# Performance work log

Hardware: AMD Instinct MI355X
Metric: run time of the kernel (lower is better)

## Reference

```python
import math
import jax, jax.numpy as jnp
import numpy as np

H = 16  # head_count
D = 1024  # model_dim
DH = D // H  # dim_per_head = 64
PAD_IDX = 1


def setup_inputs() -> dict:
    key = jax.random.key(0)
    ks = jax.random.split(key, 16)
    B, L = 4, 512
    s = 0.02
    inp = {
        'key': jax.random.normal(ks[0], (B, L, D), jnp.float32),
        'value': jax.random.normal(ks[1], (B, L, D), jnp.float32),
        'query': jax.random.normal(ks[2], (B, L, D), jnp.float32),
        'ast_parents_matrix': jax.random.randint(ks[3], (B, L, L), 0, 200, jnp.int32),
        'mask': jnp.zeros((B, 1, L), jnp.bool_),
        'Wq': jax.random.normal(ks[4], (D, D), jnp.float32) * s,
        'bq': jnp.zeros((D,), jnp.float32),
        'Wk': jax.random.normal(ks[5], (D, D), jnp.float32) * s,
        'bk': jnp.zeros((D,), jnp.float32),
        'Wv': jax.random.normal(ks[6], (D, D), jnp.float32) * s,
        'bv': jnp.zeros((D,), jnp.float32),
        'Wo': jax.random.normal(ks[7], (D, D), jnp.float32) * s,
        'bo': jnp.zeros((D,), jnp.float32),
        'struct_emb': jax.random.normal(ks[8], (200, DH), jnp.float32).at[PAD_IDX].set(0.0),
        'value_emb': jax.random.normal(ks[9], (10000, DH), jnp.float32).at[PAD_IDX].set(0.0),
    }
    return inp


def _parent_embeddings(matrix, struct_emb, value_emb):
    # matrix: (B, Lq, K) int ids; even key positions use structure vocab, odd use value vocab
    B, Lq, K = matrix.shape
    s_ids = matrix[:, :, ::2]   # (B, Lq, ceil(K/2))
    v_ids = matrix[:, :, 1::2]  # (B, Lq, floor(K/2))
    emb_s = struct_emb[s_ids]   # (B, Lq, S, DH)
    emb_v = value_emb[v_ids]    # (B, Lq, V, DH)
    S = emb_s.shape[2]
    if emb_v.shape[2] != S:  # odd K: pad value stream by one zero slot, drop after interleave
        emb_v = jnp.concatenate([emb_v, jnp.zeros_like(emb_s[:, :, :1])], axis=2)
    pe = jnp.stack([emb_s, emb_v], axis=3).reshape(B, Lq, 2 * S, DH)
    return pe[:, :, :K, :]  # (B, Lq, K, DH)


def reference(key, value, query, ast_parents_matrix, mask,
              Wq, bq, Wk, bk, Wv, bv, Wo, bo, struct_emb, value_emb):
    B, L, _ = query.shape

    def shape(x):
        return x.reshape(B, -1, H, DH).transpose(0, 2, 1, 3)  # (B,H,L,DH)

    q = shape(query @ Wq + bq) / math.sqrt(DH)
    k = shape(key @ Wk + bk)
    v = shape(value @ Wv + bv)

    qk = jnp.einsum('bhid,bhjd->bhij', q, k)  # (B,H,L,L)

    pe = _parent_embeddings(ast_parents_matrix[:, :, :L], struct_emb, value_emb)
    score_ast = jnp.einsum('bhid,bijd->bhij', q, pe)

    scores = (qk + score_ast).astype(jnp.float32)
    scores = jnp.where(mask[:, None, :, :], -1e18, scores)  # mask: (B,1,L)->(B,1,1,L)
    attn = jax.nn.softmax(scores, axis=-1).astype(q.dtype)
    # dropout p=0.0 (eval) -> identity
    context = jnp.einsum('bhij,bhjd->bhid', attn, v)  # (B,H,L,DH)
    context = context.transpose(0, 2, 1, 3).reshape(B, L, D)
    output = context @ Wo + bo
    return output, attn
```

## Files before the change

kernel.cpp:

```cpp
#include <hip/hip_runtime.h>
#include <cstddef>

#define H 16
#define D 1024
#define DH 64
#define L 512

typedef __attribute__((ext_vector_type(8))) short bf16x8;
typedef __attribute__((ext_vector_type(4))) short bf16x4;
typedef __attribute__((ext_vector_type(4))) float f32x4;

__device__ inline short f2bf(float x) {
    union { float f; unsigned u; } c; c.f = x;
    unsigned r = (c.u + 0x7FFFu + ((c.u >> 16) & 1u)) >> 16;
    return (short)r;
}
__device__ inline float bf2f(short x) {
    union { float f; unsigned u; } c;
    c.u = ((unsigned)(unsigned short)x) << 16; return c.f;
}

__device__ inline void gload_lds16(const void* g, void* l) {
    __builtin_amdgcn_global_load_lds(
        (const __attribute__((address_space(1))) unsigned int*)g,
        (__attribute__((address_space(3))) unsigned int*)l,
        16, 0, 0);
}

struct PrepArgs {
    const float* csrc[5]; short* cdst[5]; int cn[5];
    const float* W[4]; short* T[4];
};

__global__ __launch_bounds__(256) void prep_kernel(PrepArgs a) {
    const int y = blockIdx.y;
    if (y < 5) {
        const float* s = a.csrc[y];
        short* d = a.cdst[y];
        int n = a.cn[y];
        int i = (blockIdx.x * 256 + threadIdx.x) * 8;
        if (i >= n) return;
        float4 x0 = *(const float4*)(s + i);
        float4 x1 = *(const float4*)(s + i + 4);
        bf16x8 o;
        o[0] = f2bf(x0.x); o[1] = f2bf(x0.y); o[2] = f2bf(x0.z); o[3] = f2bf(x0.w);
        o[4] = f2bf(x1.x); o[5] = f2bf(x1.y); o[6] = f2bf(x1.z); o[7] = f2bf(x1.w);
        *(bf16x8*)(d + i) = o;
    } else {
        const float* W = a.W[y - 5];
        short* T = a.T[y - 5];
        int idx = blockIdx.x * 256 + threadIdx.x;
        if (idx >= 1024 * 128) return;
        int n = idx & 1023;
        int k0 = (idx >> 10) << 3;
        bf16x8 o;
        #pragma unroll
        for (int kk = 0; kk < 8; ++kk)
            o[kk] = f2bf(W[(size_t)(k0 + kk) * 1024 + n]);
        *(bf16x8*)(T + (size_t)n * 1024 + k0) = o;
    }
}

#define BM 128
#define BN 64
#define BKK 64

struct GemmBatch {
    const short* A[3]; const short* Bt[3]; const float* bias[3];
    void* out[3]; float scale[3]; int mode[3];
};

__global__ __launch_bounds__(256) void gemm_mfma_kernel(GemmBatch P, int M, int N, int K) {
    const int z = blockIdx.z;
    const short* __restrict__ A  = P.A[z];
    const short* __restrict__ Bt = P.Bt[z];
    const float* __restrict__ bias = P.bias[z];
    const float scale = P.scale[z];
    const int mode = P.mode[z];

    __shared__ short lds[(BM + BN) * BKK];
    short* As = lds;
    short* Bs = lds + BM * BKK;

    const int tid = threadIdx.x;
    const int wave = tid >> 6, lane = tid & 63;
    const int fm = lane & 15, quad = lane >> 4;
    const int m0 = blockIdx.y * BM, n0 = blockIdx.x * BN;

    int arow[4], acol[4];
    #pragma unroll
    for (int t = 0; t < 4; ++t) {
        int s = (wave * 4 + t) * 64 + lane;
        int row = s >> 3;
        int u = (s & 7) ^ (row & 7);
        arow[t] = row; acol[t] = u * 8;
    }
    int brow[2], bcol[2];
    #pragma unroll
    for (int t = 0; t < 2; ++t) {
        int s = (wave * 2 + t) * 64 + lane;
        int row = s >> 3;
        int u = (s & 7) ^ (row & 7);
        brow[t] = row; bcol[t] = u * 8;
    }

    int aoff[2][2], boff[4][2];
    #pragma unroll
    for (int mt = 0; mt < 2; ++mt)
        #pragma unroll
        for (int kst = 0; kst < 2; ++kst) {
            int row = wave * 32 + mt * 16 + fm;
            int u = quad + 4 * kst;
            aoff[mt][kst] = row * 64 + ((u ^ (row & 7)) * 8);
        }
    #pragma unroll
    for (int nt = 0; nt < 4; ++nt)
        #pragma unroll
        for (int kst = 0; kst < 2; ++kst) {
            int row = nt * 16 + fm;
            int u = quad + 4 * kst;
            boff[nt][kst] = row * 64 + ((u ^ (row & 7)) * 8);
        }

    f32x4 acc[2][4];
    #pragma unroll
    for (int mt = 0; mt < 2; ++mt)
        #pragma unroll
        for (int nt = 0; nt < 4; ++nt) acc[mt][nt] = (f32x4){0.f, 0.f, 0.f, 0.f};

    for (int k0 = 0; k0 < K; k0 += BKK) {
        __syncthreads();
        #pragma unroll
        for (int t = 0; t < 4; ++t)
            gload_lds16(A + (size_t)(m0 + arow[t]) * K + k0 + acol[t],
                        As + (wave * 4 + t) * 512);
        #pragma unroll
        for (int t = 0; t < 2; ++t)
            gload_lds16(Bt + (size_t)(n0 + brow[t]) * K + k0 + bcol[t],
                        Bs + (wave * 2 + t) * 512);
        __syncthreads();
        #pragma unroll
        for (int kst = 0; kst < 2; ++kst) {
            bf16x8 af[2], bfr[4];
            af[0] = *(const bf16x8*)(As + aoff[0][kst]);
            af[1] = *(const bf16x8*)(As + aoff[1][kst]);
            #pragma unroll
            for (int nt = 0; nt < 4; ++nt)
                bfr[nt] = *(const bf16x8*)(Bs + boff[nt][kst]);
            #pragma unroll
            for (int mt = 0; mt < 2; ++mt)
                #pragma unroll
                for (int nt = 0; nt < 4; ++nt)
                    acc[mt][nt] = __builtin_amdgcn_mfma_f32_16x16x32_bf16(
                        af[mt], bfr[nt], acc[mt][nt], 0, 0, 0);
        }
    }

    if (mode == 2) {
        __syncthreads();
        short (*T)[BM + 8] = (short(*)[BM + 8])&lds[0];
        #pragma unroll
        for (int mt = 0; mt < 2; ++mt)
            #pragma unroll
            for (int nt = 0; nt < 4; ++nt) {
                int nn = nt * 16 + fm;
                float bv = bias[n0 + nn];
                #pragma unroll
                for (int r = 0; r < 4; ++r) {
                    int mm = wave * 32 + mt * 16 + quad * 4 + r;
                    T[nn][mm] = f2bf((acc[mt][nt][r] + bv) * scale);
                }
            }
        __syncthreads();
        int b = m0 >> 9;
        int ibase = m0 & (L - 1);
        int hblk = n0 >> 6;
        int n = tid >> 2, seg = (tid & 3) * 32;
        short* dst = (short*)P.out[z] + (((size_t)(b * H + hblk) * DH + n) * L) + ibase + seg;
        #pragma unroll
        for (int c = 0; c < 4; ++c)
            *(bf16x8*)(dst + c * 8) = *(const bf16x8*)(&T[n][seg + c * 8]);
    } else {
        #pragma unroll
        for (int mt = 0; mt < 2; ++mt)
            #pragma unroll
            for (int nt = 0; nt < 4; ++nt) {
                int n = n0 + nt * 16 + fm;
                float bv = bias[n];
                #pragma unroll
                for (int r = 0; r < 4; ++r) {
                    int m = m0 + wave * 32 + mt * 16 + quad * 4 + r;
                    float val = (acc[mt][nt][r] + bv) * scale;
                    if (mode == 0) {
                        ((float*)P.out[z])[(size_t)m * N + n] = val;
                    } else {
                        int b = m >> 9, i = m & (L - 1);
                        int h = n >> 6, d = n & (DH - 1);
                        ((short*)P.out[z])[(((size_t)(b * H + h) * L + i) * DH) + d] = f2bf(val);
                    }
                }
            }
    }
}

__global__ __launch_bounds__(256) void ast_kernel(
    const short* __restrict__ Qb, const int* __restrict__ mat,
    const short* __restrict__ semb, const short* __restrict__ vemb,
    short* __restrict__ Sast)
{
    const int i = blockIdx.x, b = blockIdx.y;
    const int tid = threadIdx.x;
    const int wave = tid >> 6, lane = tid & 63;
    const int fm = lane & 15, quad = lane >> 4;
    __shared__ short Sl[H][L + 8];

    const short* qp = Qb + (((size_t)(b * H + fm) * L + i) * DH);
    bf16x8 a0 = *(const bf16x8*)(qp + quad * 8);
    bf16x8 a1 = *(const bf16x8*)(qp + 32 + quad * 8);

    const int* mrow = mat + ((size_t)b * L + i) * L;

    int idxs[8];
    const short* ebase[8];
    #pragma unroll
    for (int t = 0; t < 8; ++t) {
        int j = (wave + t * 4) * 16 + fm;
        idxs[t] = mrow[j];
    }
    #pragma unroll
    for (int t = 0; t < 8; ++t) {
        int j = (wave + t * 4) * 16 + fm;
        ebase[t] = ((j & 1) ? vemb : semb) + (size_t)idxs[t] * DH;
    }

    #pragma unroll
    for (int t = 0; t < 8; ++t) {
        int j = (wave + t * 4) * 16 + fm;
        bf16x8 b0 = *(const bf16x8*)(ebase[t] + quad * 8);
        bf16x8 b1 = *(const bf16x8*)(ebase[t] + 32 + quad * 8);
        f32x4 c = {0.f, 0.f, 0.f, 0.f};
        c = __builtin_amdgcn_mfma_f32_16x16x32_bf16(a0, b0, c, 0, 0, 0);
        c = __builtin_amdgcn_mfma_f32_16x16x32_bf16(a1, b1, c, 0, 0, 0);
        #pragma unroll
        for (int r = 0; r < 4; ++r)
            Sl[quad * 4 + r][j] = f2bf(c[r]);
    }
    __syncthreads();
    int hh = tid >> 4, j0 = (tid & 15) * 32;
    short* dst = Sast + ((((size_t)b * L + i) * H + hh) * L) + j0;
    #pragma unroll
    for (int c = 0; c < 4; ++c)
        *(bf16x8*)(dst + c * 8) = *(const bf16x8*)(&Sl[hh][j0 + c * 8]);
}

__global__ __launch_bounds__(256) void attn_fused_kernel(
    const short* __restrict__ Qb, const short* __restrict__ Kb,
    const short* __restrict__ Vt, const short* __restrict__ Sast,
    const unsigned char* __restrict__ mask,
    float* __restrict__ attn, short* __restrict__ ctx)
{
    const int i0 = blockIdx.x * 16;
    const int h = blockIdx.y;
    const int b = blockIdx.z;
    const int tid = threadIdx.x;
    const int wave = tid >> 6, lane = tid & 63;
    const int fm = lane & 15, quad = lane >> 4;

    __shared__ short Pb[16][L + 8];
    __shared__ float red_m[4][16];
    __shared__ float red_l[4][16];

    {
        int r = tid >> 4, seg = (tid & 15) * 32;
        const short* sp = Sast + ((((size_t)b * L + i0 + r) * H + h) * L) + seg;
        #pragma unroll
        for (int c = 0; c < 4; ++c)
            *(bf16x8*)(&Pb[r][seg + c * 8]) = *(const bf16x8*)(sp + c * 8);
    }

    const short* qp = Qb + (((size_t)(b * H + h) * L + i0 + fm) * DH);
    bf16x8 a0 = *(const bf16x8*)(qp + quad * 8);
    bf16x8 a1 = *(const bf16x8*)(qp + 32 + quad * 8);
    const short* Kbase = Kb + ((size_t)(b * H + h) * L) * DH;
    __syncthreads();

    float s[8][4];
    float mx[4] = {-3.0e38f, -3.0e38f, -3.0e38f, -3.0e38f};
    #pragma unroll
    for (int t = 0; t < 8; ++t) {
        int j = wave * 128 + t * 16 + fm;
        const short* kr = Kbase + (size_t)j * DH;
        bf16x8 b0 = *(const bf16x8*)(kr + quad * 8);
        bf16x8 b1 = *(const bf16x8*)(kr + 32 + quad * 8);
        f32x4 c = {0.f, 0.f, 0.f, 0.f};
        c = __builtin_amdgcn_mfma_f32_16x16x32_bf16(a0, b0, c, 0, 0, 0);
        c = __builtin_amdgcn_mfma_f32_16x16x32_bf16(a1, b1, c, 0, 0, 0);
        bool mk = mask[(size_t)b * L + j] != 0;
        #pragma unroll
        for (int r = 0; r < 4; ++r) {
            int ir = quad * 4 + r;
            float sv = c[r] + bf2f(Pb[ir][j]);
            sv = mk ? -1e18f : sv;
            s[t][r] = sv;
            mx[r] = fmaxf(mx[r], sv);
        }
    }

    #pragma unroll
    for (int off = 1; off <= 8; off <<= 1)
        #pragma unroll
        for (int r = 0; r < 4; ++r)
            mx[r] = fmaxf(mx[r], __shfl_xor(mx[r], off));
    if (fm == 0)
        #pragma unroll
        for (int r = 0; r < 4; ++r) red_m[wave][quad * 4 + r] = mx[r];
    __syncthreads();
    float M_[4];
    #pragma unroll
    for (int r = 0; r < 4; ++r) {
        int ir = quad * 4 + r;
        M_[r] = fmaxf(fmaxf(red_m[0][ir], red_m[1][ir]),
                      fmaxf(red_m[2][ir], red_m[3][ir]));
    }

    float sum[4] = {0.f, 0.f, 0.f, 0.f};
    #pragma unroll
    for (int t = 0; t < 8; ++t)
        #pragma unroll
        for (int r = 0; r < 4; ++r) {
            float e = __expf(s[t][r] - M_[r]);
            s[t][r] = e;
            sum[r] += e;
        }
    #pragma unroll
    for (int off = 1; off <= 8; off <<= 1)
        #pragma unroll
        for (int r = 0; r < 4; ++r)
            sum[r] += __shfl_xor(sum[r], off);
    if (fm == 0)
        #pragma unroll
        for (int r = 0; r < 4; ++r) red_l[wave][quad * 4 + r] = sum[r];
    __syncthreads();
    float inv[4];
    #pragma unroll
    for (int r = 0; r < 4; ++r) {
        int ir = quad * 4 + r;
        inv[r] = 1.f / (red_l[0][ir] + red_l[1][ir] + red_l[2][ir] + red_l[3][ir]);
    }

    #pragma unroll
    for (int t = 0; t < 8; ++t) {
        int j = wave * 128 + t * 16 + fm;
        #pragma unroll
        for (int r = 0; r < 4; ++r) {
            int ir = quad * 4 + r;
            Pb[ir][j] = f2bf(s[t][r] * inv[r]);
        }
    }
    __syncthreads();

    {
        int rowl = tid >> 4;
        int c0 = (tid & 15) * 8;
        float* arow = attn + (((size_t)(b * H + h) * L + i0 + rowl) * L);
        #pragma unroll
        for (int c = 0; c < 4; ++c) {
            int col = c0 + c * 128;
            bf16x8 pk = *(const bf16x8*)(&Pb[rowl][col]);
            float4 v0, v1;
            v0.x = bf2f(pk[0]); v0.y = bf2f(pk[1]); v0.z = bf2f(pk[2]); v0.w = bf2f(pk[3]);
            v1.x = bf2f(pk[4]); v1.y = bf2f(pk[5]); v1.z = bf2f(pk[6]); v1.w = bf2f(pk[7]);
            *(float4*)(arow + col) = v0;
            *(float4*)(arow + col + 4) = v1;
        }
    }

    const short* Vb = Vt + (((size_t)(b * H + h) * DH + wave * 16 + fm) * L);
    f32x4 o = {0.f, 0.f, 0.f, 0.f};
    for (int ks = 0; ks < L; ks += 32) {
        bf16x8 pa = *(const bf16x8*)(&Pb[fm][ks + quad * 8]);
        bf16x8 vb = *(const bf16x8*)(Vb + ks + quad * 8);
        o = __builtin_amdgcn_mfma_f32_16x16x32_bf16(pa, vb, o, 0, 0, 0);
    }
    #pragma unroll
    for (int r = 0; r < 4; ++r)
        ctx[((size_t)b * L + i0 + quad * 4 + r) * D + h * DH + wave * 16 + fm] = f2bf(o[r]);
}

extern "C" void kernel_launch(void* const* d_in, const int* in_sizes, int n_in,
                              void* d_out, int out_size, void* d_ws, size_t ws_size,
                              hipStream_t stream) {
    const float* key_in   = (const float*)d_in[0];
    const float* value_in = (const float*)d_in[1];
    const float* query_in = (const float*)d_in[2];
    const int*   mat      = (const int*)d_in[3];
    const unsigned char* mask = (const unsigned char*)d_in[4];
    const float* Wq = (const float*)d_in[5];
    const float* bq = (const float*)d_in[6];
    const float* Wk = (const float*)d_in[7];
    const float* bk = (const float*)d_in[8];
    const float* Wv = (const float*)d_in[9];
    const float* bv = (const float*)d_in[10];
    const float* Wo = (const float*)d_in[11];
    const float* bo = (const float*)d_in[12];
    const float* struct_emb = (const float*)d_in[13];
    const float* value_emb  = (const float*)d_in[14];

    const int B = in_sizes[2] / (L * D);
    const int M = B * L;

    short* p = (short*)d_ws;
    short* xk  = p;  p += (size_t)M * D;
    short* xv  = p;  p += (size_t)M * D;
    short* xq  = p;  p += (size_t)M * D;
    short* WqT = p;  p += (size_t)D * D;
    short* WkT = p;  p += (size_t)D * D;
    short* WvT = p;  p += (size_t)D * D;
    short* WoT = p;  p += (size_t)D * D;
    short* semb = p; p += 16384;
    short* vemb = p; p += (size_t)in_sizes[14];
    short* Qb = p;   p += (size_t)M * D;
    short* Kb = p;   p += (size_t)M * D;
    short* Vt = p;   p += (size_t)M * D;
    short* Sast = p; p += (size_t)B * L * H * L;
    short* ctx = xk;

    float* out_p  = (float*)d_out;
    float* attn_p = out_p + (size_t)M * D;

    PrepArgs pa;
    pa.csrc[0] = key_in;     pa.cdst[0] = xk;   pa.cn[0] = M * D;
    pa.csrc[1] = value_in;   pa.cdst[1] = xv;   pa.cn[1] = M * D;
    pa.csrc[2] = query_in;   pa.cdst[2] = xq;   pa.cn[2] = M * D;
    pa.csrc[3] = struct_emb; pa.cdst[3] = semb; pa.cn[3] = in_sizes[13];
    pa.csrc[4] = value_emb;  pa.cdst[4] = vemb; pa.cn[4] = in_sizes[14];
    pa.W[0] = Wq; pa.W[1] = Wk; pa.W[2] = Wv; pa.W[3] = Wo;
    pa.T[0] = WqT; pa.T[1] = WkT; pa.T[2] = WvT; pa.T[3] = WoT;
    prep_kernel<<<dim3((M * D) / 2048, 9), 256, 0, stream>>>(pa);

    GemmBatch qkv;
    qkv.A[0] = xq; qkv.Bt[0] = WqT; qkv.bias[0] = bq; qkv.out[0] = Qb; qkv.scale[0] = 0.125f; qkv.mode[0] = 1;
    qkv.A[1] = xk; qkv.Bt[1] = WkT; qkv.bias[1] = bk; qkv.out[1] = Kb; qkv.scale[1] = 1.0f;   qkv.mode[1] = 1;
    qkv.A[2] = xv; qkv.Bt[2] = WvT; qkv.bias[2] = bv; qkv.out[2] = Vt; qkv.scale[2] = 1.0f;   qkv.mode[2] = 2;
    gemm_mfma_kernel<<<dim3(D / BN, M / BM, 3), 256, 0, stream>>>(qkv, M, D, D);

    ast_kernel<<<dim3(L, B), 256, 0, stream>>>(Qb, mat, semb, vemb, Sast);

    attn_fused_kernel<<<dim3(L / 16, H, B), 256, 0, stream>>>(
        Qb, Kb, Vt, Sast, mask, attn_p, ctx);

    GemmBatch fin;
    fin.A[0] = ctx; fin.Bt[0] = WoT; fin.bias[0] = bo; fin.out[0] = out_p; fin.scale[0] = 1.0f; fin.mode[0] = 0;
    fin.A[1] = ctx; fin.Bt[1] = WoT; fin.bias[1] = bo; fin.out[1] = out_p; fin.scale[1] = 1.0f; fin.mode[1] = 0;
    fin.A[2] = ctx; fin.Bt[2] = WoT; fin.bias[2] = bo; fin.out[2] = out_p; fin.scale[2] = 1.0f; fin.mode[2] = 0;
    gemm_mfma_kernel<<<dim3(D / BN, M / BM, 1), 256, 0, stream>>>(fin, M, D, D);
}
```

Before: 240.9 us.

## Prefetch K/V fragments into registers and merge softmax reductions into one barrier

New measurement: 237.9 us. Within noise of the previous version (-1.2%).

```diff
diff --git a/kernel.cpp b/kernel.cpp
--- a/kernel.cpp
+++ b/kernel.cpp
@@ -253,7 +253,7 @@
         *(bf16x8*)(dst + c * 8) = *(const bf16x8*)(&Sl[hh][j0 + c * 8]);
 }
 
-__global__ __launch_bounds__(256) void attn_fused_kernel(
+__global__ __launch_bounds__(256, 3) void attn_fused_kernel(
     const short* __restrict__ Qb, const short* __restrict__ Kb,
     const short* __restrict__ Vt, const short* __restrict__ Sast,
     const unsigned char* __restrict__ mask,
@@ -282,6 +282,20 @@
     bf16x8 a0 = *(const bf16x8*)(qp + quad * 8);
     bf16x8 a1 = *(const bf16x8*)(qp + 32 + quad * 8);
     const short* Kbase = Kb + ((size_t)(b * H + h) * L) * DH;
+
+    bf16x8 kf[8][2];
+    #pragma unroll
+    for (int t = 0; t < 8; ++t) {
+        int j = wave * 128 + t * 16 + fm;
+        const short* kr = Kbase + (size_t)j * DH;
+        kf[t][0] = *(const bf16x8*)(kr + quad * 8);
+        kf[t][1] = *(const bf16x8*)(kr + 32 + quad * 8);
+    }
+    bool mk[8];
+    #pragma unroll
+    for (int t = 0; t < 8; ++t)
+        mk[t] = mask[(size_t)b * L + wave * 128 + t * 16 + fm] != 0;
+
     __syncthreads();
 
     float s[8][4];
@@ -289,46 +303,37 @@
     #pragma unroll
     for (int t = 0; t < 8; ++t) {
         int j = wave * 128 + t * 16 + fm;
-        const short* kr = Kbase + (size_t)j * DH;
-        bf16x8 b0 = *(const bf16x8*)(kr + quad * 8);
-        bf16x8 b1 = *(const bf16x8*)(kr + 32 + quad * 8);
         f32x4 c = {0.f, 0.f, 0.f, 0.f};
-        c = __builtin_amdgcn_mfma_f32_16x16x32_bf16(a0, b0, c, 0, 0, 0);
-        c = __builtin_amdgcn_mfma_f32_16x16x32_bf16(a1, b1, c, 0, 0, 0);
-        bool mk = mask[(size_t)b * L + j] != 0;
+        c = __builtin_amdgcn_mfma_f32_16x16x32_bf16(a0, kf[t][0], c, 0, 0, 0);
+        c = __builtin_amdgcn_mfma_f32_16x16x32_bf16(a1, kf[t][1], c, 0, 0, 0);
         #pragma unroll
         for (int r = 0; r < 4; ++r) {
             int ir = quad * 4 + r;
             float sv = c[r] + bf2f(Pb[ir][j]);
-            sv = mk ? -1e18f : sv;
+            sv = mk[t] ? -1e18f : sv;
             s[t][r] = sv;
             mx[r] = fmaxf(mx[r], sv);
         }
     }
 
+    bf16x8 vf[16];
+    const short* Vb = Vt + (((size_t)(b * H + h) * DH + wave * 16 + fm) * L);
+    #pragma unroll
+    for (int i = 0; i < 16; ++i)
+        vf[i] = *(const bf16x8*)(Vb + i * 32 + quad * 8);
+
     #pragma unroll
     for (int off = 1; off <= 8; off <<= 1)
         #pragma unroll
         for (int r = 0; r < 4; ++r)
             mx[r] = fmaxf(mx[r], __shfl_xor(mx[r], off));
-    if (fm == 0)
-        #pragma unroll
-        for (int r = 0; r < 4; ++r) red_m[wave][quad * 4 + r] = mx[r];
-    __syncthreads();
-    float M_[4];
-    #pragma unroll
-    for (int r = 0; r < 4; ++r) {
-        int ir = quad * 4 + r;
-        M_[r] = fmaxf(fmaxf(red_m[0][ir], red_m[1][ir]),
-                      fmaxf(red_m[2][ir], red_m[3][ir]));
-    }
 
     float sum[4] = {0.f, 0.f, 0.f, 0.f};
     #pragma unroll
     for (int t = 0; t < 8; ++t)
         #pragma unroll
         for (int r = 0; r < 4; ++r) {
-            float e = __expf(s[t][r] - M_[r]);
+            float e = __expf(s[t][r] - mx[r]);
             s[t][r] = e;
             sum[r] += e;
         }
@@ -339,13 +344,24 @@
             sum[r] += __shfl_xor(sum[r], off);
     if (fm == 0)
         #pragma unroll
-        for (int r = 0; r < 4; ++r) red_l[wave][quad * 4 + r] = sum[r];
+        for (int r = 0; r < 4; ++r) {
+            red_m[wave][quad * 4 + r] = mx[r];
+            red_l[wave][quad * 4 + r] = sum[r];
+        }
     __syncthreads();
-    float inv[4];
+
+    float fac[4];
     #pragma unroll
     for (int r = 0; r < 4; ++r) {
         int ir = quad * 4 + r;
-        inv[r] = 1.f / (red_l[0][ir] + red_l[1][ir] + red_l[2][ir] + red_l[3][ir]);
+        float m0_ = red_m[0][ir], m1_ = red_m[1][ir];
+        float m2_ = red_m[2][ir], m3_ = red_m[3][ir];
+        float M_ = fmaxf(fmaxf(m0_, m1_), fmaxf(m2_, m3_));
+        float T_ = red_l[0][ir] * __expf(m0_ - M_)
+                 + red_l[1][ir] * __expf(m1_ - M_)
+                 + red_l[2][ir] * __expf(m2_ - M_)
+                 + red_l[3][ir] * __expf(m3_ - M_);
+        fac[r] = __expf(mx[r] - M_) / T_;
     }
 
     #pragma unroll
@@ -354,7 +370,7 @@
         #pragma unroll
         for (int r = 0; r < 4; ++r) {
             int ir = quad * 4 + r;
-            Pb[ir][j] = f2bf(s[t][r] * inv[r]);
+            Pb[ir][j] = f2bf(s[t][r] * fac[r]);
         }
     }
     __syncthreads();
@@ -375,12 +391,11 @@
         }
     }
 
-    const short* Vb = Vt + (((size_t)(b * H + h) * DH + wave * 16 + fm) * L);
     f32x4 o = {0.f, 0.f, 0.f, 0.f};
-    for (int ks = 0; ks < L; ks += 32) {
-        bf16x8 pa = *(const bf16x8*)(&Pb[fm][ks + quad * 8]);
-        bf16x8 vb = *(const bf16x8*)(Vb + ks + quad * 8);
-        o = __builtin_amdgcn_mfma_f32_16x16x32_bf16(pa, vb, o, 0, 0, 0);
+    #pragma unroll
+    for (int i = 0; i < 16; ++i) {
+        bf16x8 pa = *(const bf16x8*)(&Pb[fm][i * 32 + quad * 8]);
+        o = __builtin_amdgcn_mfma_f32_16x16x32_bf16(pa, vf[i], o, 0, 0, 0);
     }
     #pragma unroll
     for (int r = 0; r < 4; ++r)
```

## Enlarge GEMM tile to 128x128 and restructure attention so each wave owns full rows

Applied to the files above, without the earlier changes.

Result: slower. 252.2 us (+4.7%).

```diff
diff --git a/kernel.cpp b/kernel.cpp
--- a/kernel.cpp
+++ b/kernel.cpp
@@ -62,7 +62,7 @@
 }
 
 #define BM 128
-#define BN 64
+#define BN 128
 #define BKK 64
 
 struct GemmBatch {
@@ -78,38 +78,31 @@
     const float scale = P.scale[z];
     const int mode = P.mode[z];
 
-    __shared__ short lds[(BM + BN) * BKK];
+    __shared__ short lds[17408];
     short* As = lds;
-    short* Bs = lds + BM * BKK;
+    short* Bs = lds + 8192;
 
     const int tid = threadIdx.x;
     const int wave = tid >> 6, lane = tid & 63;
     const int fm = lane & 15, quad = lane >> 4;
+    const int wr = wave >> 1, wc = wave & 1;
     const int m0 = blockIdx.y * BM, n0 = blockIdx.x * BN;
 
-    int arow[4], acol[4];
+    int srow[4], scol[4];
     #pragma unroll
     for (int t = 0; t < 4; ++t) {
         int s = (wave * 4 + t) * 64 + lane;
         int row = s >> 3;
         int u = (s & 7) ^ (row & 7);
-        arow[t] = row; acol[t] = u * 8;
-    }
-    int brow[2], bcol[2];
-    #pragma unroll
-    for (int t = 0; t < 2; ++t) {
-        int s = (wave * 2 + t) * 64 + lane;
-        int row = s >> 3;
-        int u = (s & 7) ^ (row & 7);
-        brow[t] = row; bcol[t] = u * 8;
-    }
-
-    int aoff[2][2], boff[4][2];
-    #pragma unroll
-    for (int mt = 0; mt < 2; ++mt)
+        srow[t] = row; scol[t] = u * 8;
+    }
+
+    int aoff[4][2], boff[4][2];
+    #pragma unroll
+    for (int mt = 0; mt < 4; ++mt)
         #pragma unroll
         for (int kst = 0; kst < 2; ++kst) {
-            int row = wave * 32 + mt * 16 + fm;
+            int row = wr * 64 + mt * 16 + fm;
             int u = quad + 4 * kst;
             aoff[mt][kst] = row * 64 + ((u ^ (row & 7)) * 8);
         }
@@ -117,14 +110,14 @@
     for (int nt = 0; nt < 4; ++nt)
         #pragma unroll
         for (int kst = 0; kst < 2; ++kst) {
-            int row = nt * 16 + fm;
+            int row = wc * 64 + nt * 16 + fm;
             int u = quad + 4 * kst;
             boff[nt][kst] = row * 64 + ((u ^ (row & 7)) * 8);
         }
 
-    f32x4 acc[2][4];
-    #pragma unroll
-    for (int mt = 0; mt < 2; ++mt)
+    f32x4 acc[4][4];
+    #pragma unroll
+    for (int mt = 0; mt < 4; ++mt)
         #pragma unroll
         for (int nt = 0; nt < 4; ++nt) acc[mt][nt] = (f32x4){0.f, 0.f, 0.f, 0.f};
 
@@ -132,23 +125,24 @@
         __syncthreads();
         #pragma unroll
         for (int t = 0; t < 4; ++t)
-            gload_lds16(A + (size_t)(m0 + arow[t]) * K + k0 + acol[t],
+            gload_lds16(A + (size_t)(m0 + srow[t]) * K + k0 + scol[t],
                         As + (wave * 4 + t) * 512);
         #pragma unroll
-        for (int t = 0; t < 2; ++t)
-            gload_lds16(Bt + (size_t)(n0 + brow[t]) * K + k0 + bcol[t],
-                        Bs + (wave * 2 + t) * 512);
+        for (int t = 0; t < 4; ++t)
+            gload_lds16(Bt + (size_t)(n0 + srow[t]) * K + k0 + scol[t],
+                        Bs + (wave * 4 + t) * 512);
         __syncthreads();
         #pragma unroll
         for (int kst = 0; kst < 2; ++kst) {
-            bf16x8 af[2], bfr[4];
-            af[0] = *(const bf16x8*)(As + aoff[0][kst]);
-            af[1] = *(const bf16x8*)(As + aoff[1][kst]);
+            bf16x8 af[4], bfr[4];
+            #pragma unroll
+            for (int mt = 0; mt < 4; ++mt)
+                af[mt] = *(const bf16x8*)(As + aoff[mt][kst]);
             #pragma unroll
             for (int nt = 0; nt < 4; ++nt)
                 bfr[nt] = *(const bf16x8*)(Bs + boff[nt][kst]);
             #pragma unroll
-            for (int mt = 0; mt < 2; ++mt)
+            for (int mt = 0; mt < 4; ++mt)
                 #pragma unroll
                 for (int nt = 0; nt < 4; ++nt)
                     acc[mt][nt] = __builtin_amdgcn_mfma_f32_16x16x32_bf16(
@@ -158,45 +152,45 @@
 
     if (mode == 2) {
         __syncthreads();
-        short (*T)[BM + 8] = (short(*)[BM + 8])&lds[0];
-        #pragma unroll
-        for (int mt = 0; mt < 2; ++mt)
+        short (*T)[136] = (short(*)[136])&lds[0];
+        #pragma unroll
+        for (int mt = 0; mt < 4; ++mt)
             #pragma unroll
             for (int nt = 0; nt < 4; ++nt) {
-                int nn = nt * 16 + fm;
+                int nn = wc * 64 + nt * 16 + fm;
                 float bv = bias[n0 + nn];
                 #pragma unroll
                 for (int r = 0; r < 4; ++r) {
-                    int mm = wave * 32 + mt * 16 + quad * 4 + r;
+                    int mm = wr * 64 + mt * 16 + quad * 4 + r;
                     T[nn][mm] = f2bf((acc[mt][nt][r] + bv) * scale);
                 }
             }
         __syncthreads();
         int b = m0 >> 9;
         int ibase = m0 & (L - 1);
-        int hblk = n0 >> 6;
-        int n = tid >> 2, seg = (tid & 3) * 32;
-        short* dst = (short*)P.out[z] + (((size_t)(b * H + hblk) * DH + n) * L) + ibase + seg;
-        #pragma unroll
-        for (int c = 0; c < 4; ++c)
-            *(bf16x8*)(dst + c * 8) = *(const bf16x8*)(&T[n][seg + c * 8]);
+        int n = tid >> 1, half = tid & 1;
+        int hh = (n0 + n) >> 6, d = n & 63;
+        short* dst = (short*)P.out[z] + (((size_t)(b * H + hh) * DH + d) * L) + ibase + half * 64;
+        #pragma unroll
+        for (int c = 0; c < 8; ++c)
+            *(bf16x8*)(dst + c * 8) = *(const bf16x8*)(&T[n][half * 64 + c * 8]);
     } else {
         #pragma unroll
-        for (int mt = 0; mt < 2; ++mt)
+        for (int mt = 0; mt < 4; ++mt)
             #pragma unroll
             for (int nt = 0; nt < 4; ++nt) {
-                int n = n0 + nt * 16 + fm;
+                int n = n0 + wc * 64 + nt * 16 + fm;
                 float bv = bias[n];
                 #pragma unroll
                 for (int r = 0; r < 4; ++r) {
-                    int m = m0 + wave * 32 + mt * 16 + quad * 4 + r;
+                    int m = m0 + wr * 64 + mt * 16 + quad * 4 + r;
                     float val = (acc[mt][nt][r] + bv) * scale;
                     if (mode == 0) {
                         ((float*)P.out[z])[(size_t)m * N + n] = val;
                     } else {
                         int b = m >> 9, i = m & (L - 1);
-                        int h = n >> 6, d = n & (DH - 1);
-                        ((short*)P.out[z])[(((size_t)(b * H + h) * L + i) * DH) + d] = f2bf(val);
+                        int h = n >> 6, dd = n & (DH - 1);
+                        ((short*)P.out[z])[(((size_t)(b * H + h) * L + i) * DH) + dd] = f2bf(val);
                     }
                 }
             }
@@ -253,138 +247,113 @@
         *(bf16x8*)(dst + c * 8) = *(const bf16x8*)(&Sl[hh][j0 + c * 8]);
 }
 
-__global__ __launch_bounds__(256) void attn_fused_kernel(
+#define PPITCH 520
+
+__global__ __launch_bounds__(256, 2) void attn_fused_kernel(
     const short* __restrict__ Qb, const short* __restrict__ Kb,
     const short* __restrict__ Vt, const short* __restrict__ Sast,
     const unsigned char* __restrict__ mask,
     float* __restrict__ attn, short* __restrict__ ctx)
 {
-    const int i0 = blockIdx.x * 16;
+    const int i0 = blockIdx.x * 64;
     const int h = blockIdx.y;
     const int b = blockIdx.z;
     const int tid = threadIdx.x;
     const int wave = tid >> 6, lane = tid & 63;
     const int fm = lane & 15, quad = lane >> 4;
 
-    __shared__ short Pb[16][L + 8];
-    __shared__ float red_m[4][16];
-    __shared__ float red_l[4][16];
+    __shared__ short Pb[64 * PPITCH];
 
     {
-        int r = tid >> 4, seg = (tid & 15) * 32;
-        const short* sp = Sast + ((((size_t)b * L + i0 + r) * H + h) * L) + seg;
-        #pragma unroll
-        for (int c = 0; c < 4; ++c)
-            *(bf16x8*)(&Pb[r][seg + c * 8]) = *(const bf16x8*)(sp + c * 8);
-    }
-
-    const short* qp = Qb + (((size_t)(b * H + h) * L + i0 + fm) * DH);
-    bf16x8 a0 = *(const bf16x8*)(qp + quad * 8);
-    bf16x8 a1 = *(const bf16x8*)(qp + 32 + quad * 8);
+        const short* base = Sast + (((size_t)b * L + i0) * H + h) * L;
+        #pragma unroll
+        for (int p = 0; p < 16; ++p) {
+            int row = p * 4 + (tid >> 6);
+            int col = (tid & 63) * 8;
+            *(bf16x8*)(&Pb[row * PPITCH + col]) =
+                *(const bf16x8*)(base + (size_t)row * (H * L) + col);
+        }
+    }
+
+    const int iw = i0 + wave * 16;
+    const short* qp = Qb + (((size_t)(b * H + h) * L + iw + fm) * DH);
+    bf16x8 q0 = *(const bf16x8*)(qp + quad * 8);
+    bf16x8 q1 = *(const bf16x8*)(qp + 32 + quad * 8);
     const short* Kbase = Kb + ((size_t)(b * H + h) * L) * DH;
+    const unsigned char* mrow = mask + (size_t)b * L;
+
     __syncthreads();
 
-    float s[8][4];
-    float mx[4] = {-3.0e38f, -3.0e38f, -3.0e38f, -3.0e38f};
-    #pragma unroll
-    for (int t = 0; t < 8; ++t) {
-        int j = wave * 128 + t * 16 + fm;
-        const short* kr = Kbase + (size_t)j * DH;
-        bf16x8 b0 = *(const bf16x8*)(kr + quad * 8);
-        bf16x8 b1 = *(const bf16x8*)(kr + 32 + quad * 8);
+    short* Prow = &Pb[(wave * 16 + fm) * PPITCH];
+
+    float s[32][4];
+    float mx = -3.0e38f;
+    #pragma unroll
+    for (int t = 0; t < 32; ++t) {
+        const short* kr = Kbase + (size_t)(t * 16 + fm) * DH;
+        bf16x8 k0 = *(const bf16x8*)(kr + quad * 8);
+        bf16x8 k1 = *(const bf16x8*)(kr + 32 + quad * 8);
         f32x4 c = {0.f, 0.f, 0.f, 0.f};
-        c = __builtin_amdgcn_mfma_f32_16x16x32_bf16(a0, b0, c, 0, 0, 0);
-        c = __builtin_amdgcn_mfma_f32_16x16x32_bf16(a1, b1, c, 0, 0, 0);
-        bool mk = mask[(size_t)b * L + j] != 0;
+        c = __builtin_amdgcn_mfma_f32_16x16x32_bf16(k0, q0, c, 0, 0, 0);
+        c = __builtin_amdgcn_mfma_f32_16x16x32_bf16(k1, q1, c, 0, 0, 0);
+        bf16x4 sa = *(const bf16x4*)(&Prow[t * 16 + quad * 4]);
+        unsigned mku = *(const unsigned*)(mrow + t * 16 + quad * 4);
         #pragma unroll
         for (int r = 0; r < 4; ++r) {
-            int ir = quad * 4 + r;
-            float sv = c[r] + bf2f(Pb[ir][j]);
-            sv = mk ? -1e18f : sv;
+            float sv = c[r] + bf2f(sa[r]);
+            sv = ((mku >> (8 * r)) & 255u) ? -1e18f : sv;
             s[t][r] = sv;
-            mx[r] = fmaxf(mx[r], sv);
-        }
-    }
-
-    #pragma unroll
-    for (int off = 1; off <= 8; off <<= 1)
+            mx = fmaxf(mx, sv);
+        }
+    }
+
+    mx = fmaxf(mx, __shfl_xor(mx, 16));
+    mx = fmaxf(mx, __shfl_xor(mx, 32));
+
+    float sum = 0.f;
+    #pragma unroll
+    for (int t = 0; t < 32; ++t)
+        #pragma unroll
+        for (int r = 0; r < 4; ++r) {
+            float e = __expf(s[t][r] - mx);
+            s[t][r] = e;
+            sum += e;
+        }
+    sum += __shfl_xor(sum, 16);
+    sum += __shfl_xor(sum, 32);
+    float inv = 1.f / sum;
+
+    float* arow = attn + (((size_t)(b * H + h) * L + iw + fm) * L);
+    #pragma unroll
+    for (int t = 0; t < 32; ++t) {
+        bf16x4 pw;
         #pragma unroll
         for (int r = 0; r < 4; ++r)
-            mx[r] = fmaxf(mx[r], __shfl_xor(mx[r], off));
-    if (fm == 0)
-        #pragma unroll
-        for (int r = 0; r < 4; ++r) red_m[wave][quad * 4 + r] = mx[r];
-    __syncthreads();
-    float M_[4];
-    #pragma unroll
-    for (int r = 0; r < 4; ++r) {
-        int ir = quad * 4 + r;
-        M_[r] = fmaxf(fmaxf(red_m[0][ir], red_m[1][ir]),
-                      fmaxf(red_m[2][ir], red_m[3][ir]));
-    }
-
-    float sum[4] = {0.f, 0.f, 0.f, 0.f};
-    #pragma unroll
-    for (int t = 0; t < 8; ++t)
-        #pragma unroll
-        for (int r = 0; r < 4; ++r) {
-            float e = __expf(s[t][r] - M_[r]);
-            s[t][r] = e;
-            sum[r] += e;
-        }
-    #pragma unroll
-    for (int off = 1; off <= 8; off <<= 1)
+            pw[r] = f2bf(s[t][r] * inv);
+        *(bf16x4*)(&Prow[t * 16 + quad * 4]) = pw;
+        float4 v;
+        v.x = bf2f(pw[0]); v.y = bf2f(pw[1]); v.z = bf2f(pw[2]); v.w = bf2f(pw[3]);
+        *(float4*)(arow + t * 16 + quad * 4) = v;
+    }
+
+    const short* Vbase = Vt + ((size_t)(b * H + h) * DH) * L;
+    f32x4 o[4];
+    #pragma unroll
+    for (int dt = 0; dt < 4; ++dt) o[dt] = (f32x4){0.f, 0.f, 0.f, 0.f};
+    #pragma unroll
+    for (int ks = 0; ks < L; ks += 32) {
+        bf16x8 pa = *(const bf16x8*)(&Prow[ks + quad * 8]);
+        #pragma unroll
+        for (int dt = 0; dt < 4; ++dt) {
+            bf16x8 vb = *(const bf16x8*)(Vbase + (size_t)(dt * 16 + fm) * L + ks + quad * 8);
+            o[dt] = __builtin_amdgcn_mfma_f32_16x16x32_bf16(pa, vb, o[dt], 0, 0, 0);
+        }
+    }
+    #pragma unroll
+    for (int dt = 0; dt < 4; ++dt)
         #pragma unroll
         for (int r = 0; r < 4; ++r)
-            sum[r] += __shfl_xor(sum[r], off);
-    if (fm == 0)
-        #pragma unroll
-        for (int r = 0; r < 4; ++r) red_l[wave][quad * 4 + r] = sum[r];
-    __syncthreads();
-    float inv[4];
-    #pragma unroll
-    for (int r = 0; r < 4; ++r) {
-        int ir = quad * 4 + r;
-        inv[r] = 1.f / (red_l[0][ir] + red_l[1][ir] + red_l[2][ir] + red_l[3][ir]);
-    }
-
-    #pragma unroll
-    for (int t = 0; t < 8; ++t) {
-        int j = wave * 128 + t * 16 + fm;
-        #pragma unroll
-        for (int r = 0; r < 4; ++r) {
-            int ir = quad * 4 + r;
-            Pb[ir][j] = f2bf(s[t][r] * inv[r]);
-        }
-    }
-    __syncthreads();
-
-    {
-        int rowl = tid >> 4;
-        int c0 = (tid & 15) * 8;
-        float* arow = attn + (((size_t)(b * H + h) * L + i0 + rowl) * L);
-        #pragma unroll
-        for (int c = 0; c < 4; ++c) {
-            int col = c0 + c * 128;
-            bf16x8 pk = *(const bf16x8*)(&Pb[rowl][col]);
-            float4 v0, v1;
-            v0.x = bf2f(pk[0]); v0.y = bf2f(pk[1]); v0.z = bf2f(pk[2]); v0.w = bf2f(pk[3]);
-            v1.x = bf2f(pk[4]); v1.y = bf2f(pk[5]); v1.z = bf2f(pk[6]); v1.w = bf2f(pk[7]);
-            *(float4*)(arow + col) = v0;
-            *(float4*)(arow + col + 4) = v1;
-        }
-    }
-
-    const short* Vb = Vt + (((size_t)(b * H + h) * DH + wave * 16 + fm) * L);
-    f32x4 o = {0.f, 0.f, 0.f, 0.f};
-    for (int ks = 0; ks < L; ks += 32) {
-        bf16x8 pa = *(const bf16x8*)(&Pb[fm][ks + quad * 8]);
-        bf16x8 vb = *(const bf16x8*)(Vb + ks + quad * 8);
-        o = __builtin_amdgcn_mfma_f32_16x16x32_bf16(pa, vb, o, 0, 0, 0);
-    }
-    #pragma unroll
-    for (int r = 0; r < 4; ++r)
-        ctx[((size_t)b * L + i0 + quad * 4 + r) * D + h * DH + wave * 16 + fm] = f2bf(o[r]);
+            ctx[((size_t)b * L + iw + quad * 4 + r) * D + h * DH + dt * 16 + fm] = f2bf(o[dt][r]);
 }
 
 extern "C" void kernel_launch(void* const* d_in, const int* in_sizes, int n_in,
@@ -446,7 +415,7 @@
 
     ast_kernel<<<dim3(L, B), 256, 0, stream>>>(Qb, mat, semb, vemb, Sast);
 
-    attn_fused_kernel<<<dim3(L / 16, H, B), 256, 0, stream>>>(
+    attn_fused_kernel<<<dim3(L / 64, H, B), 256, 0, stream>>>(
         Qb, Kb, Vt, Sast, mask, attn_p, ctx);
 
     GemmBatch fin;
```
